# Optimization experiments

Hardware: AMD Instinct MI355X
Metric: run time of the kernel (lower is better)

## Reference

```python
import jax, jax.numpy as jnp
import numpy as np

B, T, DE, DD, A, FN, FS = 32, 2000, 512, 1024, 128, 32, 16
TEMPERATURE = 1.0


def setup_inputs() -> dict:
    key = jax.random.key(0)
    ks = jax.random.split(key, 10)
    input_enc = jax.random.normal(ks[0], (B, T, DE), dtype=jnp.float32)
    # lengths in [T//2, T] so no zero-length utterances
    enc_lengths = jax.random.randint(ks[1], (B,), T // 2, T + 1, dtype=jnp.int32)
    input_dec = jax.random.normal(ks[2], (B, DD), dtype=jnp.float32)
    # prev_att: previous-step attention weights (masked, normalized)
    prev_att = jax.random.uniform(ks[3], (B, T), dtype=jnp.float32)
    pad = jnp.arange(T)[None, :] >= enc_lengths[:, None]
    prev_att = jnp.where(pad, 0.0, prev_att)
    prev_att = prev_att / jnp.sum(prev_att, axis=1, keepdims=True)
    # parameters
    conv_w = jax.random.normal(ks[4], (FN, 1, 2 * FS + 1), dtype=jnp.float32) * 0.1  # [out,in,k]
    enc_w = jax.random.normal(ks[5], (A, DE), dtype=jnp.float32) * 0.04
    dec_w = jax.random.normal(ks[6], (A, DD), dtype=jnp.float32) * 0.03
    att_w = jax.random.normal(ks[7], (A, FN), dtype=jnp.float32) * 0.17
    att_b = jnp.zeros((A,), dtype=jnp.float32)
    out_w = jax.random.normal(ks[8], (1, A), dtype=jnp.float32) * 0.09
    return dict(input_enc=input_enc, enc_lengths=enc_lengths, input_dec=input_dec,
                prev_att=prev_att, conv_w=conv_w, enc_w=enc_w, dec_w=dec_w,
                att_w=att_w, att_b=att_b, out_w=out_w)


def reference(input_enc, enc_lengths, input_dec, prev_att,
              conv_w, enc_w, dec_w, att_w, att_b, out_w):
    b, t, _ = input_enc.shape
    fs = (conv_w.shape[-1] - 1) // 2  # 'same' padding
    # padding mask: True at padded positions t >= length
    mask = jnp.arange(t)[None, :] >= enc_lengths[:, None]  # [B,T]
    # location features: Conv1d over prev attention, 1 -> FN channels, same length
    conv = jax.lax.conv_general_dilated(
        prev_att[:, None, :], conv_w, window_strides=(1,),
        padding=[(fs, fs)], dimension_numbers=("NCH", "OIH", "NCH"))  # [B,FN,T]
    loc_feat = conv.transpose(0, 2, 1)  # [B,T,FN]
    projected_att = loc_feat @ att_w.T + att_b        # [B,T,A]
    projected_enc = input_enc @ enc_w.T               # [B,T,A]
    projected_dec = (input_dec @ dec_w.T)[:, None, :]  # [B,1,A]
    score = jnp.squeeze(jnp.tanh(projected_att + projected_enc + projected_dec) @ out_w.T, -1)  # [B,T]
    score = jnp.where(mask, -jnp.inf, score)
    att_weight = jax.nn.softmax(TEMPERATURE * score, axis=1)  # [B,T]
    context = jnp.einsum("btd,bt->bd", input_enc, att_weight)  # [B,DE]
    return context, att_weight
```

## Files before the change

kernel.cpp:

```cpp
#include <hip/hip_runtime.h>
#include <hip/hip_bf16.h>
#include <math.h>

#define B_ 32
#define T_ 2000
#define DE_ 512
#define DD_ 1024
#define A_ 128
#define FN_ 32
#define FS_ 16
#define KW_ (2*FS_+1)

typedef __bf16 bf16x8 __attribute__((ext_vector_type(8)));
typedef __bf16 bf16x4 __attribute__((ext_vector_type(4)));
typedef float f32x4 __attribute__((ext_vector_type(4)));

#define BT 64
#define KC 32
#define LSTR 40

__device__ __forceinline__ void load_lds16(const void* g, void* l) {
    __builtin_amdgcn_global_load_lds(
        (const __attribute__((address_space(1))) unsigned int*)g,
        (__attribute__((address_space(3))) unsigned int*)l, 16, 0, 0);
}

__device__ __forceinline__ bf16x8 cvt8v(f32x4 x, f32x4 y) {
    bf16x8 o;
    o[0] = (__bf16)x[0]; o[1] = (__bf16)x[1]; o[2] = (__bf16)x[2]; o[3] = (__bf16)x[3];
    o[4] = (__bf16)y[0]; o[5] = (__bf16)y[1]; o[6] = (__bf16)y[2]; o[7] = (__bf16)y[3];
    return o;
}

__global__ __launch_bounds__(256) void prep_kernel(
    const float* __restrict__ enc_w, const float* __restrict__ att_w,
    const float* __restrict__ input_dec, const float* __restrict__ dec_w,
    const float* __restrict__ att_b,
    __bf16* __restrict__ enc_bf, __bf16* __restrict__ att_bf,
    float* __restrict__ pdec, float* __restrict__ ctx_un )
{
    int bx = blockIdx.x, tid = threadIdx.x;
    if (bx < 64) {
        int i = bx * 256 + tid;
        float4 v = ((const float4*)enc_w)[i];
        bf16x4 o;
        o[0] = (__bf16)v.x; o[1] = (__bf16)v.y; o[2] = (__bf16)v.z; o[3] = (__bf16)v.w;
        *(bf16x4*)(enc_bf + (size_t)i * 4) = o;
        if (i < (A_ * FN_) / 4) {
            float4 w = ((const float4*)att_w)[i];
            bf16x4 p;
            p[0] = (__bf16)w.x; p[1] = (__bf16)w.y; p[2] = (__bf16)w.z; p[3] = (__bf16)w.w;
            *(bf16x4*)(att_bf + (size_t)i * 4) = p;
        }
    } else if (bx < 192) {
        int pb = bx - 64;
        int b  = pb >> 2;
        int a0 = (pb & 3) * 32;
        int al = tid >> 3;
        int kg = tid & 7;
        int a  = a0 + al;
        const float4* w = (const float4*)(dec_w + (size_t)a * DD_);
        const float4* x = (const float4*)(input_dec + (size_t)b * DD_);
        float acc = 0.f;
        #pragma unroll 8
        for (int j = 0; j < 32; j++) {
            int i4 = kg + j * 8;
            float4 wv = w[i4], xv = x[i4];
            acc += wv.x * xv.x + wv.y * xv.y + wv.z * xv.z + wv.w * xv.w;
        }
        acc += __shfl_xor(acc, 1, 64);
        acc += __shfl_xor(acc, 2, 64);
        acc += __shfl_xor(acc, 4, 64);
        if (kg == 0) pdec[b * A_ + a] = acc + att_b[a];
    } else {
        int idx = (bx - 192) * 256 + tid;
        if (idx < (B_ * DE_ + B_) / 4 + 1)
            ((float4*)ctx_un)[idx] = make_float4(0.f, 0.f, 0.f, 0.f);
    }
}

__global__ __launch_bounds__(256, 4) void score_kernel(
    const float* __restrict__ input_enc, const __bf16* __restrict__ enc_bf,
    const float* __restrict__ prev_att,  const float* __restrict__ conv_w,
    const __bf16* __restrict__ att_bf,   const float* __restrict__ pdec,
    const float* __restrict__ out_w,     const int* __restrict__ lengths,
    float* __restrict__ wbuf, float* __restrict__ ctx_un,
    float* __restrict__ denom)
{
    __shared__ __align__(16) char At[2][8192];
    __shared__ __align__(16) char Bt[2][8192];
    __shared__ __align__(16) float pa_s[BT + 2 * FS_];
    __shared__ __align__(16) __bf16 loc_s[BT * LSTR];
    __shared__ float w_s[BT];

    const int tid  = threadIdx.x;
    const int lane = tid & 63;
    const int wv   = tid >> 6;
    const int b  = blockIdx.y;
    const int t0 = blockIdx.x * BT;
    const int len = lengths[b];

    if (t0 >= len) {
        if (tid < BT) {
            int t = t0 + tid;
            if (t < T_) wbuf[b * T_ + t] = 0.f;
        }
        return;
    }

    auto issueA = [&](int kc, int bufi) {
        #pragma unroll
        for (int j = 0; j < 2; j++) {
            int s  = j * 256 + tid;
            int r  = s >> 3;
            int q  = s & 7;
            int cl = q ^ (r & 7);
            int t  = t0 + r; if (t > T_ - 1) t = T_ - 1;
            load_lds16(input_enc + ((size_t)(b * T_ + t)) * DE_ + kc + cl * 4,
                       At[bufi] + j * 4096 + wv * 1024);
        }
    };
    auto issueB = [&](int kc, int bufi) {
        #pragma unroll
        for (int j = 0; j < 2; j++) {
            int s  = j * 256 + tid;
            int r  = s >> 2;
            int q  = s & 3;
            int cl = q ^ ((r >> 1) & 3);
            load_lds16(enc_bf + (size_t)r * DE_ + kc + cl * 8,
                       Bt[bufi] + j * 4096 + wv * 1024);
        }
    };

    issueA(0, 0);   issueB(0, 0);
    issueA(KC, 1);  issueB(KC, 1);

    const int f    = tid & 31;
    const int rblk = tid >> 5;
    float cwr[KW_];
    #pragma unroll
    for (int k = 0; k < KW_; k++) cwr[k] = conv_w[f * KW_ + k];

    if (tid < BT + 2 * FS_) {
        int t = t0 - FS_ + tid;
        pa_s[tid] = (t >= 0 && t < T_) ? prev_att[b * T_ + t] : 0.f;
    }
    __syncthreads();

    {
        float par[40];
        #pragma unroll
        for (int j = 0; j < 10; j++)
            *(float4*)&par[j * 4] = *(const float4*)&pa_s[rblk * 8 + j * 4];
        float accv[8] = {0.f, 0.f, 0.f, 0.f, 0.f, 0.f, 0.f, 0.f};
        #pragma unroll
        for (int k = 0; k < KW_; k++) {
            float c = cwr[k];
            #pragma unroll
            for (int j = 0; j < 8; j++) accv[j] += par[j + k] * c;
        }
        #pragma unroll
        for (int j = 0; j < 8; j++)
            loc_s[(rblk * 8 + j) * LSTR + f] = (__bf16)accv[j];
    }
    __syncthreads();

    const int col  = lane & 15;
    const int grp  = lane >> 4;
    const int rowb = wv * 16 + col;
    const int keyA = rowb & 7;

    f32x4 acc[8];
    const f32x4 zero = (f32x4){0.f, 0.f, 0.f, 0.f};

    {
        bf16x8 afrag = *(const bf16x8*)(loc_s + rowb * LSTR + grp * 8);
        #pragma unroll
        for (int i = 0; i < 8; i++) {
            bf16x8 bfrag = *(const bf16x8*)(att_bf + (size_t)(i * 16 + col) * FN_ + grp * 8);
            acc[i] = __builtin_amdgcn_mfma_f32_16x16x32_bf16(afrag, bfrag, zero, 0, 0, 0);
        }
    }

    auto compute = [&](const char* Ab, const char* Bb) {
        f32x4 v0 = *(const f32x4*)(Ab + rowb * 128 + ((grp * 2)     ^ keyA) * 16);
        f32x4 v1 = *(const f32x4*)(Ab + rowb * 128 + ((grp * 2 + 1) ^ keyA) * 16);
        bf16x8 af = cvt8v(v0, v1);
        #pragma unroll
        for (int i = 0; i < 8; i++) {
            int row = i * 16 + col;
            bf16x8 bfrag = *(const bf16x8*)(Bb + row * 64 + ((grp ^ ((row >> 1) & 3)) * 16));
            acc[i] = __builtin_amdgcn_mfma_f32_16x16x32_bf16(af, bfrag, acc[i], 0, 0, 0);
        }
    };

    #pragma unroll
    for (int it = 0; it < 16; ++it) {
        compute(At[it & 1], Bt[it & 1]);
        if (it == 15) break;
        __builtin_amdgcn_s_barrier();
        if (it + 2 < 16) {
            issueA((it + 2) * KC, it & 1);
            issueB((it + 2) * KC, it & 1);
            asm volatile("s_waitcnt vmcnt(4)" ::: "memory");
        } else {
            asm volatile("s_waitcnt vmcnt(0)" ::: "memory");
        }
        __builtin_amdgcn_s_barrier();
    }

    float s[4] = {0.f, 0.f, 0.f, 0.f};
    float Mabs = 0.f;
    #pragma unroll
    for (int i = 0; i < 8; i++) {
        int a = i * 16 + col;
        float ow = out_w[a];
        Mabs += fabsf(ow);
        float bias = pdec[b * A_ + a];
        #pragma unroll
        for (int r = 0; r < 4; r++) {
            float v = acc[i][r] + bias;
            v = fminf(fmaxf(v, -15.f), 15.f);
            float e = __expf(2.f * v);
            s[r] += ow * ((e - 1.f) / (e + 1.f));
        }
    }
    #pragma unroll
    for (int r = 0; r < 4; r++) {
        s[r] += __shfl_xor(s[r], 1, 64);
        s[r] += __shfl_xor(s[r], 2, 64);
        s[r] += __shfl_xor(s[r], 4, 64);
        s[r] += __shfl_xor(s[r], 8, 64);
    }
    Mabs += __shfl_xor(Mabs, 1, 64);
    Mabs += __shfl_xor(Mabs, 2, 64);
    Mabs += __shfl_xor(Mabs, 4, 64);
    Mabs += __shfl_xor(Mabs, 8, 64);

    if (col == 0) {
        #pragma unroll
        for (int r = 0; r < 4; r++) {
            int rl = wv * 16 + grp * 4 + r;
            int t = t0 + rl;
            float w = 0.f;
            if (t < len) w = __expf(s[r] - Mabs);
            w_s[rl] = w;
            if (t < T_) wbuf[b * T_ + t] = w;
        }
    }
    __syncthreads();

    if (tid < 64) {
        float w = w_s[tid];
        w += __shfl_xor(w, 1, 64);
        w += __shfl_xor(w, 2, 64);
        w += __shfl_xor(w, 4, 64);
        w += __shfl_xor(w, 8, 64);
        w += __shfl_xor(w, 16, 64);
        w += __shfl_xor(w, 32, 64);
        if (tid == 0) atomicAdd(&denom[b], w);
    }

    int n_eff = len - t0;
    if (n_eff > BT) n_eff = BT;
    if (n_eff > 0) {
        int d0 = tid * 2;
        const float* ebase = input_enc + ((size_t)(b * T_ + t0)) * DE_ + d0;
        float cx = 0.f, cy = 0.f;
        #pragma unroll 8
        for (int t = 0; t < n_eff; t++) {
            float w = w_s[t];
            float2 v = *(const float2*)(ebase + (size_t)t * DE_);
            cx += w * v.x;
            cy += w * v.y;
        }
        atomicAdd(&ctx_un[b * DE_ + d0 + 0], cx);
        atomicAdd(&ctx_un[b * DE_ + d0 + 1], cy);
    }
}

__global__ __launch_bounds__(256) void finalize_kernel(
    const float* __restrict__ wbuf, const float* __restrict__ ctx_un,
    const float* __restrict__ denom, float* __restrict__ out)
{
    int bx = blockIdx.x, tid = threadIdx.x;
    if (bx < 64) {
        int i4 = bx * 256 + tid;
        if (i4 < (B_ * T_) / 4) {
            int b = i4 / (T_ / 4);
            float inv = 1.f / denom[b];
            float4 w = ((const float4*)wbuf)[i4];
            w.x *= inv; w.y *= inv; w.z *= inv; w.w *= inv;
            ((float4*)(out + B_ * DE_))[i4] = w;
        }
    } else {
        int j = (bx - 64) * 256 + tid;
        int b = j / (DE_ / 4);
        float inv = 1.f / denom[b];
        float4 c = ((const float4*)ctx_un)[j];
        c.x *= inv; c.y *= inv; c.z *= inv; c.w *= inv;
        ((float4*)out)[j] = c;
    }
}

extern "C" void kernel_launch(void* const* d_in, const int* in_sizes, int n_in,
                              void* d_out, int out_size, void* d_ws, size_t ws_size,
                              hipStream_t stream)
{
    const float* input_enc   = (const float*)d_in[0];
    const int*   enc_lengths = (const int*)d_in[1];
    const float* input_dec   = (const float*)d_in[2];
    const float* prev_att    = (const float*)d_in[3];
    const float* conv_w      = (const float*)d_in[4];
    const float* enc_w       = (const float*)d_in[5];
    const float* dec_w       = (const float*)d_in[6];
    const float* att_w       = (const float*)d_in[7];
    const float* att_b       = (const float*)d_in[8];
    const float* out_w       = (const float*)d_in[9];

    float* out = (float*)d_out;
    char* ws = (char*)d_ws;
    float*  pdec   = (float*)ws;
    float*  wbuf   = (float*)(ws + 16384);
    __bf16* enc_bf = (__bf16*)(ws + 272384);
    __bf16* att_bf = (__bf16*)(ws + 403456);
    float*  ctx_un = (float*)(ws + 411648);
    float*  denom  = (float*)(ws + 477184);

    prep_kernel<<<209, 256, 0, stream>>>(enc_w, att_w, input_dec, dec_w, att_b,
                                         enc_bf, att_bf, pdec, ctx_un);

    dim3 sgrid((T_ + BT - 1) / BT, B_);
    score_kernel<<<sgrid, 256, 0, stream>>>(input_enc, enc_bf, prev_att, conv_w,
                                            att_bf, pdec, out_w, enc_lengths,
                                            wbuf, ctx_un, denom);

    finalize_kernel<<<80, 256, 0, stream>>>(wbuf, ctx_un, denom, out);
}
```

Before: 223.8 us.

## Move context reduction into finalize kernel and replace atomics with per-block partials

The weighted context sum over the encoder leaves the score kernel and moves into the finalize kernel, which re-reads input_enc per batch across 256 blocks with a shared-memory reduction instead of global atomics. The softmax denominator becomes per-block partial slots summed in finalize, so the context and denom zeroing in prep goes away. This removes atomic contention and shortens the score kernel's tail. The cost is a second full pass over input_enc (about 131MB) that the score kernel's cache may no longer hold, and each finalize block now loops serially over up to 2000 timesteps.

```diff
diff --git a/kernel.cpp b/kernel.cpp
--- a/kernel.cpp
+++ b/kernel.cpp
@@ -10,6 +10,7 @@
 #define FN_ 32
 #define FS_ 16
 #define KW_ (2*FS_+1)
+#define NBX 32
 
 typedef __bf16 bf16x8 __attribute__((ext_vector_type(8)));
 typedef __bf16 bf16x4 __attribute__((ext_vector_type(4)));
@@ -37,7 +38,7 @@
     const float* __restrict__ input_dec, const float* __restrict__ dec_w,
     const float* __restrict__ att_b,
     __bf16* __restrict__ enc_bf, __bf16* __restrict__ att_bf,
-    float* __restrict__ pdec, float* __restrict__ ctx_un )
+    float* __restrict__ pdec)
 {
     int bx = blockIdx.x, tid = threadIdx.x;
     if (bx < 64) {
@@ -52,7 +53,7 @@
             p[0] = (__bf16)w.x; p[1] = (__bf16)w.y; p[2] = (__bf16)w.z; p[3] = (__bf16)w.w;
             *(bf16x4*)(att_bf + (size_t)i * 4) = p;
         }
-    } else if (bx < 192) {
+    } else {
         int pb = bx - 64;
         int b  = pb >> 2;
         int a0 = (pb & 3) * 32;
@@ -72,10 +73,6 @@
         acc += __shfl_xor(acc, 2, 64);
         acc += __shfl_xor(acc, 4, 64);
         if (kg == 0) pdec[b * A_ + a] = acc + att_b[a];
-    } else {
-        int idx = (bx - 192) * 256 + tid;
-        if (idx < (B_ * DE_ + B_) / 4 + 1)
-            ((float4*)ctx_un)[idx] = make_float4(0.f, 0.f, 0.f, 0.f);
     }
 }
 
@@ -84,8 +81,7 @@
     const float* __restrict__ prev_att,  const float* __restrict__ conv_w,
     const __bf16* __restrict__ att_bf,   const float* __restrict__ pdec,
     const float* __restrict__ out_w,     const int* __restrict__ lengths,
-    float* __restrict__ wbuf, float* __restrict__ ctx_un,
-    float* __restrict__ denom)
+    float* __restrict__ wbuf, float* __restrict__ dpart)
 {
     __shared__ __align__(16) char At[2][8192];
     __shared__ __align__(16) char Bt[2][8192];
@@ -97,14 +93,17 @@
     const int lane = tid & 63;
     const int wv   = tid >> 6;
     const int b  = blockIdx.y;
-    const int t0 = blockIdx.x * BT;
+    const int bx = blockIdx.x;
+    const int t0 = bx * BT;
     const int len = lengths[b];
+    const int slot = b * NBX + bx;
 
     if (t0 >= len) {
         if (tid < BT) {
             int t = t0 + tid;
             if (t < T_) wbuf[b * T_ + t] = 0.f;
         }
+        if (tid == 0) dpart[slot] = 0.f;
         return;
     }
 
@@ -258,48 +257,51 @@
         w += __shfl_xor(w, 8, 64);
         w += __shfl_xor(w, 16, 64);
         w += __shfl_xor(w, 32, 64);
-        if (tid == 0) atomicAdd(&denom[b], w);
-    }
-
-    int n_eff = len - t0;
-    if (n_eff > BT) n_eff = BT;
-    if (n_eff > 0) {
-        int d0 = tid * 2;
-        const float* ebase = input_enc + ((size_t)(b * T_ + t0)) * DE_ + d0;
-        float cx = 0.f, cy = 0.f;
-        #pragma unroll 8
-        for (int t = 0; t < n_eff; t++) {
-            float w = w_s[t];
-            float2 v = *(const float2*)(ebase + (size_t)t * DE_);
-            cx += w * v.x;
-            cy += w * v.y;
-        }
-        atomicAdd(&ctx_un[b * DE_ + d0 + 0], cx);
-        atomicAdd(&ctx_un[b * DE_ + d0 + 1], cy);
+        if (tid == 0) dpart[slot] = w;
     }
 }
 
 __global__ __launch_bounds__(256) void finalize_kernel(
-    const float* __restrict__ wbuf, const float* __restrict__ ctx_un,
-    const float* __restrict__ denom, float* __restrict__ out)
+    const float* __restrict__ wbuf, const float* __restrict__ input_enc,
+    const int* __restrict__ lengths, const float* __restrict__ dpart,
+    float* __restrict__ out)
 {
     int bx = blockIdx.x, tid = threadIdx.x;
     if (bx < 64) {
         int i4 = bx * 256 + tid;
         if (i4 < (B_ * T_) / 4) {
             int b = i4 / (T_ / 4);
-            float inv = 1.f / denom[b];
+            float dsum = 0.f;
+            #pragma unroll
+            for (int s = 0; s < NBX; s++) dsum += dpart[b * NBX + s];
+            float inv = 1.f / dsum;
             float4 w = ((const float4*)wbuf)[i4];
             w.x *= inv; w.y *= inv; w.z *= inv; w.w *= inv;
             ((float4*)(out + B_ * DE_))[i4] = w;
         }
     } else {
-        int j = (bx - 64) * 256 + tid;
-        int b = j / (DE_ / 4);
-        float inv = 1.f / denom[b];
-        float4 c = ((const float4*)ctx_un)[j];
-        c.x *= inv; c.y *= inv; c.z *= inv; c.w *= inv;
-        ((float4*)out)[j] = c;
+        __shared__ float red[4][64];
+        int cb  = bx - 64;
+        int b   = cb >> 3;
+        int d0  = (cb & 7) * 64;
+        int col = tid & 63;
+        int tg  = tid >> 6;
+        int len = lengths[b];
+        float dsum = 0.f;
+        #pragma unroll
+        for (int s = 0; s < NBX; s++) dsum += dpart[b * NBX + s];
+        float inv = 1.f / dsum;
+        const float* eb = input_enc + (size_t)(b * T_) * DE_ + d0 + col;
+        const float* wb = wbuf + b * T_;
+        float c = 0.f;
+        for (int t = tg; t < len; t += 4)
+            c += wb[t] * eb[(size_t)t * DE_];
+        red[tg][col] = c;
+        __syncthreads();
+        if (tg == 0) {
+            float v = red[0][col] + red[1][col] + red[2][col] + red[3][col];
+            out[b * DE_ + d0 + col] = v * inv;
+        }
     }
 }
 
@@ -324,16 +326,16 @@
     float*  wbuf   = (float*)(ws + 16384);
     __bf16* enc_bf = (__bf16*)(ws + 272384);
     __bf16* att_bf = (__bf16*)(ws + 403456);
-    float*  ctx_un = (float*)(ws + 411648);
-    float*  denom  = (float*)(ws + 477184);
-
-    prep_kernel<<<209, 256, 0, stream>>>(enc_w, att_w, input_dec, dec_w, att_b,
-                                         enc_bf, att_bf, pdec, ctx_un);
-
-    dim3 sgrid((T_ + BT - 1) / BT, B_);
+    float*  dpart  = (float*)(ws + 411648);
+
+    prep_kernel<<<192, 256, 0, stream>>>(enc_w, att_w, input_dec, dec_w, att_b,
+                                         enc_bf, att_bf, pdec);
+
+    dim3 sgrid(NBX, B_);
     score_kernel<<<sgrid, 256, 0, stream>>>(input_enc, enc_bf, prev_att, conv_w,
                                             att_bf, pdec, out_w, enc_lengths,
-                                            wbuf, ctx_un, denom);
-
-    finalize_kernel<<<80, 256, 0, stream>>>(wbuf, ctx_un, denom, out);
-}
+                                            wbuf, dpart);
+
+    finalize_kernel<<<320, 256, 0, stream>>>(wbuf, input_enc, enc_lengths,
+                                             dpart, out);
+}
```

Measured after the change: 335.3 us. 1.5x slower.
